# Performance work log

Hardware: AMD Instinct MI355X
Metric: run time of the kernel (lower is better)

The kernel has to match this reference:

```python
import jax, jax.numpy as jnp
import numpy as np

IN_DIM, DIM, H, L, B, N = 20, 128, 8, 3, 2, 192
DH = DIM // H
EPS = 1e-5


def _conv1d(x, w):
    # x: [b, Cin, n], w: [Cout, Cin, 3], pad=1
    return jax.lax.conv_general_dilated(x, w, (1,), [(1, 1)], dimension_numbers=('NCH', 'OIH', 'NCH'))


def _conv2d(x, w):
    # x: [b, Cin, n, n], w: [Cout, Cin, 3, 3], pad=1
    return jax.lax.conv_general_dilated(x, w, (1, 1), [(1, 1), (1, 1)], dimension_numbers=('NCHW', 'OIHW', 'NCHW'))


def _bn(x, g, b, axes):
    # BatchNorm in training mode (batch statistics, biased variance), channel axis = 1
    m = jnp.mean(x, axes, keepdims=True)
    v = jnp.var(x, axes, keepdims=True)
    sh = [1] * x.ndim
    sh[1] = -1
    return (x - m) / jnp.sqrt(v + EPS) * g.reshape(sh) + b.reshape(sh)


def _ln(x, g, b):
    m = jnp.mean(x, -1, keepdims=True)
    v = jnp.var(x, -1, keepdims=True)
    return (x - m) / jnp.sqrt(v + EPS) * g + b


def _seq2pair(c):
    # c: [b, C, n] -> [b, 2C, n, n]; first C channels constant over j, second C constant over i
    b, C, n = c.shape
    a = jnp.broadcast_to(c[:, :, :, None], (b, C, n, n))
    p = jnp.broadcast_to(c[:, :, None, :], (b, C, n, n))
    return jnp.concatenate([a, p], axis=1)


def _forward(seq, mask, conv1_w, conv2_w, ln_g, ln_b, c1d_w, bn1_g, bn1_b, c2d_w, bn2_g, bn2_b,
             wq_w, wq_b, wk_w, wk_b, wv_w, wv_b, wd_w, wd_b, wl_w, wl_b, fc_w, fc_b):
    b, n, _ = seq.shape
    s = seq.transpose(0, 2, 1)                    # [b, in_dim, n]
    x = _conv1d(s, conv1_w).transpose(0, 2, 1)    # [b, n, dim]
    c = _conv1d(s, conv2_w)                       # [b, dim, n]
    c2 = _seq2pair(c)                             # [b, 2*dim, n, n]
    scale = jnp.sqrt(jnp.asarray(DH, x.dtype))
    m4 = mask[:, None, None, :]                   # [b, 1, 1, n]
    for i in range(L):
        c = jax.nn.relu(_bn(_conv1d(c, c1d_w[i]), bn1_g[i], bn1_b[i], (0, 2)))
        x = _ln(x + c.transpose(0, 2, 1), ln_g[i], ln_b[i])
        c2 = c2 + _seq2pair(c)
        c2 = jax.nn.relu(_bn(_conv2d(c2, c2d_w[i]), bn2_g[i], bn2_b[i], (0, 2, 3)))
        dsym = c2 + c2.transpose(0, 1, 3, 2)      # symmetric pair features [b, 2*dim, n, n]
        gate = jax.nn.sigmoid(jnp.einsum('bcij,hc->bhij', dsym, wd_w[i]) + wd_b[i][None, :, None, None])
        heads = lambda y: y.reshape(b, n, H, DH).transpose(0, 2, 1, 3)
        q = heads(jax.nn.relu(x @ wq_w[i].T + wq_b[i]))
        k = heads(jax.nn.relu(x @ wk_w[i].T + wk_b[i]))
        v = heads(jax.nn.relu(x @ wv_w[i].T + wv_b[i]))
        a = jnp.einsum('bhid,bhjd->bhij', q, k) / scale
        e = jnp.exp(a - jnp.max(a, -1, keepdims=True)) * m4   # hand-rolled masked softmax
        attn = e / (jnp.sum(e, -1, keepdims=True) + 1e-6)
        attn = attn * gate                        # post-softmax multiplicative pair bias
        upd = jnp.einsum('bhij,bhjd->bhid', attn, v).transpose(0, 2, 1, 3).reshape(b, n, DIM)
        x = jax.nn.relu((x + upd) @ wl_w[i].T + wl_b[i])   # dropout = identity (eval)
    return jax.nn.relu(x @ fc_w.T + fc_b)


def setup_inputs():
    key = jax.random.key(0)
    ks = jax.random.split(key, 16)
    rn = lambda k, shape, s=0.05: jax.random.normal(k, shape, jnp.float32) * s
    C2 = 2 * DIM
    return {
        'seq': jax.random.normal(ks[0], (B, N, IN_DIM), jnp.float32),
        'mask': (jax.random.uniform(ks[1], (B, N)) > 0.1).astype(jnp.float32),
        'conv1_w': rn(ks[2], (DIM, IN_DIM, 3)),
        'conv2_w': rn(ks[3], (DIM, IN_DIM, 3)),
        'ln_g': jnp.ones((L, DIM), jnp.float32),
        'ln_b': jnp.zeros((L, DIM), jnp.float32),
        'c1d_w': rn(ks[4], (L, DIM, DIM, 3)),
        'bn1_g': jnp.ones((L, DIM), jnp.float32),
        'bn1_b': jnp.zeros((L, DIM), jnp.float32),
        'c2d_w': rn(ks[5], (L, C2, C2, 3, 3), 0.02),
        'bn2_g': jnp.ones((L, C2), jnp.float32),
        'bn2_b': jnp.zeros((L, C2), jnp.float32),
        'wq_w': rn(ks[6], (L, DIM, DIM)), 'wq_b': jnp.zeros((L, DIM), jnp.float32),
        'wk_w': rn(ks[7], (L, DIM, DIM)), 'wk_b': jnp.zeros((L, DIM), jnp.float32),
        'wv_w': rn(ks[8], (L, DIM, DIM)), 'wv_b': jnp.zeros((L, DIM), jnp.float32),
        'wd_w': rn(ks[9], (L, H, C2)), 'wd_b': jnp.zeros((L, H), jnp.float32),
        'wl_w': rn(ks[10], (L, DIM, DIM)), 'wl_b': jnp.zeros((L, DIM), jnp.float32),
        'fc_w': rn(ks[11], (DIM, DIM)), 'fc_b': jnp.zeros((DIM,), jnp.float32),
    }


def reference(seq, mask, conv1_w, conv2_w, ln_g, ln_b, c1d_w, bn1_g, bn1_b, c2d_w, bn2_g, bn2_b,
              wq_w, wq_b, wk_w, wk_b, wv_w, wv_b, wd_w, wd_b, wl_w, wl_b, fc_w, fc_b):
    return _forward(seq, mask, conv1_w, conv2_w, ln_g, ln_b, c1d_w, bn1_g, bn1_b, c2d_w, bn2_g, bn2_b,
                    wq_w, wq_b, wk_w, wk_b, wv_w, wv_b, wd_w, wd_b, wl_w, wl_b, fc_w, fc_b)
```

## Files before the change

kernel.cpp:

```cpp
#include <hip/hip_runtime.h>
#include <math.h>

#define IN_DIM 20
#define DIM 128
#define HH 8
#define LL 3
#define BB 2
#define NP 192
#define DHH 16
#define C2 256
#define NN (NP*NP)
#define EPS 1e-5f

#define PR 200
#define PC 224

typedef __bf16 bf16x8 __attribute__((ext_vector_type(8)));
typedef float  f32x16 __attribute__((ext_vector_type(16)));

union Pack8 { __bf16 h[8]; uint4 u; };

#define GLOAD16(gp, lp) \
  __builtin_amdgcn_global_load_lds((const __attribute__((address_space(1))) uint4*)(gp), \
                                   (__attribute__((address_space(3))) uint4*)(lp), 16, 0, 0)

__global__ void k_conv_init(const float* __restrict__ seq, const float* __restrict__ w1,
                            const float* __restrict__ w2, float* __restrict__ X,
                            float* __restrict__ Cc, float* __restrict__ CcT) {
  int t = blockIdx.x, b = blockIdx.y, oc = threadIdx.x;
  __shared__ float ss[3][IN_DIM];
  if (threadIdx.x < 3*IN_DIM) {
    int k = threadIdx.x / IN_DIM, ic = threadIdx.x % IN_DIM;
    int tt = t + k - 1;
    ss[k][ic] = (tt >= 0 && tt < NP) ? seq[(b*NP + tt)*IN_DIM + ic] : 0.f;
  }
  __syncthreads();
  float a1 = 0.f, a2 = 0.f;
  #pragma unroll
  for (int ic = 0; ic < IN_DIM; ic++) {
    #pragma unroll
    for (int k = 0; k < 3; k++) {
      float sv = ss[k][ic];
      a1 = fmaf(w1[(oc*IN_DIM + ic)*3 + k], sv, a1);
      a2 = fmaf(w2[(oc*IN_DIM + ic)*3 + k], sv, a2);
    }
  }
  X[(b*NP + t)*DIM + oc] = a1;
  Cc[(b*DIM + oc)*NP + t] = a2;
  CcT[(size_t)(b*NP + t)*DIM + oc] = a2;
}

__global__ __launch_bounds__(768)
void k_conv1d_bn_relu(const float* __restrict__ cin, const float* __restrict__ w,
                      const float* __restrict__ g, const float* __restrict__ bb,
                      float* __restrict__ cout, float* __restrict__ coutT) {
  int oc = blockIdx.x;
  int tid = threadIdx.x;
  int t = tid % NP;
  int sub = tid / NP;
  int b = sub & 1, ih = sub >> 1;
  float acc = 0.f;
  for (int ic = ih*64; ic < ih*64 + 64; ic++) {
    const float* cr = cin + (b*DIM + ic)*NP;
    const float* wr = w + (oc*DIM + ic)*3;
    float lf = (t > 0)      ? cr[t-1] : 0.f;
    float mf = cr[t];
    float rf = (t < NP-1)   ? cr[t+1] : 0.f;
    acc = fmaf(lf, wr[0], acc);
    acc = fmaf(mf, wr[1], acc);
    acc = fmaf(rf, wr[2], acc);
  }
  __shared__ float sp[4][NP];
  __shared__ float sb[768];
  sp[sub][t] = acc;
  __syncthreads();
  float raw = sp[b][t] + sp[2 + b][t];
  sb[tid] = (sub < 2) ? raw : raw * raw;
  __syncthreads();
  for (int s = 192; s >= 3; s >>= 1) {
    if (tid < s) sb[tid] += sb[tid + s];
    int u = tid - 384;
    if (u >= 0 && u < s) sb[tid] += sb[tid + s];
    __syncthreads();
  }
  float mean = (sb[0] + sb[1] + sb[2]) / 384.f;
  float var  = (sb[384] + sb[385] + sb[386]) / 384.f - mean*mean;
  float rstd = rsqrtf(var + EPS);
  if (sub < 2) {
    float v = fmaxf((raw - mean)*rstd*g[oc] + bb[oc], 0.f);
    cout[(b*DIM + oc)*NP + t] = v;
    coutT[(size_t)(b*NP + t)*DIM + oc] = v;
  }
}

__global__ void k_wtrans(const float* __restrict__ wq, const float* __restrict__ wk,
                         const float* __restrict__ wv, const float* __restrict__ wl,
                         const float* __restrict__ fcw,
                         float* __restrict__ wqt, float* __restrict__ wkt,
                         float* __restrict__ wvt, float* __restrict__ wlt,
                         float* __restrict__ fct) {
  int m = blockIdx.y;
  const float* src; float* dst;
  if (m < 3)       { src = wq + (size_t)m*DIM*DIM;     dst = wqt + (size_t)m*DIM*DIM; }
  else if (m < 6)  { src = wk + (size_t)(m-3)*DIM*DIM; dst = wkt + (size_t)(m-3)*DIM*DIM; }
  else if (m < 9)  { src = wv + (size_t)(m-6)*DIM*DIM; dst = wvt + (size_t)(m-6)*DIM*DIM; }
  else if (m < 12) { src = wl + (size_t)(m-9)*DIM*DIM; dst = wlt + (size_t)(m-9)*DIM*DIM; }
  else             { src = fcw;                        dst = fct; }
  int tile = blockIdx.x;
  int ti = tile >> 2, tj = tile & 3;
  int r = threadIdx.x >> 3, c4 = threadIdx.x & 7;
  __shared__ float t[32][33];
  float4 v = *(const float4*)(src + (ti*32 + r)*DIM + tj*32 + c4*4);
  t[r][c4*4+0] = v.x; t[r][c4*4+1] = v.y; t[r][c4*4+2] = v.z; t[r][c4*4+3] = v.w;
  __syncthreads();
  float4 o;
  o.x = t[c4*4+0][r]; o.y = t[c4*4+1][r]; o.z = t[c4*4+2][r]; o.w = t[c4*4+3][r];
  *(float4*)(dst + (tj*32 + r)*DIM + ti*32 + c4*4) = o;
}

__global__ __launch_bounds__(384)
void k_lnqkv(float* __restrict__ X, const float* __restrict__ ccT,
             const float* __restrict__ g, const float* __restrict__ bb,
             const float* __restrict__ wqt, const float* __restrict__ bq,
             const float* __restrict__ wkt, const float* __restrict__ bk,
             const float* __restrict__ wvt, const float* __restrict__ bv,
             float* __restrict__ Q, float* __restrict__ K, float* __restrict__ V) {
  int t = blockIdx.x, b = blockIdx.y;
  int tid = threadIdx.x;
  int lane = tid & 63, wave = tid >> 6;
  __shared__ float sy[DIM];
  __shared__ float sred[2];
  size_t o = (size_t)(b*NP + t)*DIM;
  float v = 0.f;
  if (tid < DIM) v = X[o + tid] + ccT[o + tid];
  if (tid < DIM) {
    float s = v;
    #pragma unroll
    for (int m = 32; m > 0; m >>= 1) s += __shfl_xor(s, m);
    if (lane == 0) sred[wave] = s;
  }
  __syncthreads();
  float mean = (sred[0] + sred[1]) * (1.f/128.f);
  float dv = v - mean;
  __syncthreads();
  if (tid < DIM) {
    float q = dv*dv;
    #pragma unroll
    for (int m = 32; m > 0; m >>= 1) q += __shfl_xor(q, m);
    if (lane == 0) sred[wave] = q;
  }
  __syncthreads();
  float var = (sred[0] + sred[1]) * (1.f/128.f);
  float rstd = rsqrtf(var + EPS);
  if (tid < DIM) {
    float xn = dv * rstd * g[tid] + bb[tid];
    X[o + tid] = xn;
    sy[tid] = xn;
  }
  __syncthreads();
  {
    int d2 = tid & 127, m = tid >> 7;
    const float* wt_m = (m == 0) ? wqt : (m == 1) ? wkt : wvt;
    const float* b_m  = (m == 0) ? bq  : (m == 1) ? bk  : bv;
    float* out_m      = (m == 0) ? Q   : (m == 1) ? K   : V;
    float acc = b_m[d2];
    for (int ee = 0; ee < DIM; ee++) acc = fmaf(wt_m[ee*DIM + d2], sy[ee], acc);
    int h = d2 >> 4, dh = d2 & 15;
    out_m[((size_t)(b*HH + h)*NP + t)*DHH + dh] = fmaxf(acc, 0.f);
  }
}

__global__ void k_wprep(const float* __restrict__ w, __bf16* __restrict__ wtb) {
  int l = blockIdx.x / C2, oc = blockIdx.x % C2;
  int tid = threadIdx.x;
  __shared__ float swt[C2*9];
  const float4* wsrc = (const float4*)(w + ((size_t)(l*C2 + oc))*C2*9);
  for (int idx = tid; idx < 576; idx += 256) ((float4*)swt)[idx] = wsrc[idx];
  __syncthreads();
  for (int v = tid; v < 288; v += 256) {
    int chunk = v / 18, rem = v % 18;
    int kk = rem >> 1, kh = rem & 1;
    Pack8 p;
    #pragma unroll
    for (int e = 0; e < 8; e++)
      p.h[e] = (__bf16)swt[(chunk*16 + kh*8 + e)*9 + kk];
    size_t unit = ((((size_t)(l*16 + chunk)*9 + kk)*2 + kh)*256 + oc);
    ((uint4*)wtb)[unit] = p.u;
  }
}

__global__ void k_make_convin(const float* __restrict__ CcT, const float* __restrict__ CLT0,
                              __bf16* __restrict__ inb, float* __restrict__ STATALL) {
  int idx = blockIdx.x*256 + threadIdx.x;
  if (blockIdx.x == 0) {
    for (int z = threadIdx.x; z < 3*2*C2; z += 256) STATALL[z] = 0.f;
  }
  int kh = idx & 1;
  int t = idx >> 1;
  int gcol = t % PC; int t2 = t / PC;
  int grow = t2 % PR; int t3 = t2 / PR;
  int chunk = t3 & 15; int b = t3 >> 4;
  int i = grow - 1, j = gcol - 8;
  Pack8 p;
  if ((unsigned)i < 192u && (unsigned)j < 192u) {
    int cbase = chunk*16 + kh*8;
    const float* pa;
    const float* pb;
    if (cbase < DIM) {
      pa = CcT  + (size_t)(b*NP + i)*DIM + cbase;
      pb = CLT0 + (size_t)(b*NP + i)*DIM + cbase;
    } else {
      pa = CcT  + (size_t)(b*NP + j)*DIM + (cbase - DIM);
      pb = CLT0 + (size_t)(b*NP + j)*DIM + (cbase - DIM);
    }
    #pragma unroll
    for (int e = 0; e < 8; e++) p.h[e] = (__bf16)(pa[e] + pb[e]);
  } else {
    #pragma unroll
    for (int e = 0; e < 8; e++) p.h[e] = (__bf16)0.f;
  }
  ((uint4*)inb)[idx] = p.u;
}

__global__ __launch_bounds__(256, 2)
void k_conv2d_mfma(const __bf16* __restrict__ inb,
                   const __bf16* __restrict__ wtb,
                   __bf16* __restrict__ rawb,
                   float* __restrict__ STAT2) {
  __shared__ __align__(16) uint4 sbuf[2*2176];
  int tid = threadIdx.x;
  int jt = blockIdx.x, it = blockIdx.y, zz = blockIdx.z;
  int b = zz >> 3, oct = zz & 7;
  int i0 = it*8, j0 = jt*64, oc0 = oct*32;
  int lane = tid & 63, wv = tid >> 6;
  int ln31 = lane & 31, khl = lane >> 5;

  const uint4* gW = (const uint4*)wtb;
  const uint4* gI = (const uint4*)inb;

  f32x16 acc[2][2];
  #pragma unroll
  for (int r = 0; r < 2; r++)
    #pragma unroll
    for (int n = 0; n < 2; n++)
      #pragma unroll
      for (int q = 0; q < 16; q++) acc[r][n][q] = 0.f;

  const uint4* gp[9];
  int lofs[9];
  int gstride[9];
  bool gvalid[9];
  #pragma unroll
  for (int t = 0; t < 9; t++) {
    int L = t*4 + wv;
    gvalid[t] = (L < 34);
    if (L < 9) {
      int u = L*64 + lane;
      int kkh = u >> 5;
      int ocl = u & 31;
      gp[t] = gW + (size_t)kkh*256 + oc0 + ocl;
      lofs[t] = u;
      gstride[t] = 4608;
    } else {
      int u = L*64 + lane - 576;
      int r = u / 160;
      int rem = u % 160;
      int kh = rem / 80;
      int c = rem % 80;
      gp[t] = gI + (((size_t)(b*16)*PR) + i0 + r)*PC*2 + (size_t)(j0 + c)*2 + kh;
      lofs[t] = 576 + u;
      gstride[t] = PR*PC*2;
    }
  }

  auto issue = [&](int buf) {
    uint4* lbase = sbuf + buf*2176;
    #pragma unroll
    for (int t = 0; t < 9; t++) {
      if (gvalid[t]) {
        GLOAD16(gp[t], lbase + lofs[t]);
        gp[t] += gstride[t];
      }
    }
  };

  issue(0);

  for (int chunk = 0; chunk < 16; ++chunk) {
    int buf = chunk & 1;
    __syncthreads();
    if (chunk < 15) issue(buf ^ 1);
    const __bf16* Wl = (const __bf16*)(sbuf + buf*2176);
    const __bf16* Il = (const __bf16*)(sbuf + buf*2176 + 576);
    #pragma unroll
    for (int kj = 0; kj < 3; kj++) {
      bf16x8 bfr[4][2];
      #pragma unroll
      for (int rr = 0; rr < 4; rr++) {
        int r = wv*2 + rr;
        #pragma unroll
        for (int ch = 0; ch < 2; ch++) {
          int c = ch*32 + ln31 + kj + 7;
          bfr[rr][ch] = *(const bf16x8*)(Il + ((r*2 + khl)*80 + c)*8);
        }
      }
      #pragma unroll
      for (int ki = 0; ki < 3; ki++) {
        int kk = ki*3 + kj;
        bf16x8 a = *(const bf16x8*)(Wl + ((kk*2 + khl)*32 + ln31)*8);
        #pragma unroll
        for (int row = 0; row < 2; row++)
          #pragma unroll
          for (int ch = 0; ch < 2; ch++)
            acc[row][ch] = __builtin_amdgcn_mfma_f32_32x32x16_bf16(a, bfr[row + ki][ch], acc[row][ch], 0, 0, 0);
      }
    }
  }

  __syncthreads();
  float* trAll = (float*)sbuf;
  float* tr = trAll + wv*(32*33);
  float* sstat = trAll + 4*32*33;
  if (tid < 64) sstat[tid] = 0.f;
  __syncthreads();

  #pragma unroll
  for (int reg = 0; reg < 16; reg++) {
    float v00 = acc[0][0][reg], v01 = acc[0][1][reg];
    float v10 = acc[1][0][reg], v11 = acc[1][1][reg];
    float s = v00 + v01 + v10 + v11;
    float s2 = v00*v00 + v01*v01 + v10*v10 + v11*v11;
    #pragma unroll
    for (int msk = 1; msk <= 16; msk <<= 1) { s += __shfl_xor(s, msk); s2 += __shfl_xor(s2, msk); }
    if (ln31 == 0) {
      int oc_l = (reg & 3) + 8*(reg >> 2) + 4*khl;
      atomicAdd(&sstat[oc_l], s);
      atomicAdd(&sstat[32 + oc_l], s2);
    }
  }

  int Gb = oc0 >> 3;
  uint4* RAWu = (uint4*)rawb;
  #pragma unroll
  for (int row = 0; row < 2; row++) {
    int i = i0 + wv*2 + row;
    #pragma unroll
    for (int ch = 0; ch < 2; ch++) {
      #pragma unroll
      for (int reg = 0; reg < 16; reg++) {
        int r = (reg & 3) + 8*(reg >> 2) + 4*khl;
        tr[r*33 + ln31] = acc[row][ch][reg];
      }
      __builtin_amdgcn_s_waitcnt(0);
      #pragma unroll
      for (int gs = 0; gs < 2; gs++) {
        int g = khl + gs*2;
        Pack8 p;
        #pragma unroll
        for (int e = 0; e < 8; e++) p.h[e] = (__bf16)tr[(g*8 + e)*33 + ln31];
        RAWu[((size_t)(b*32 + Gb + g)*192 + i)*192 + j0 + ch*32 + ln31] = p.u;
      }
      __builtin_amdgcn_s_waitcnt(0);
    }
  }

  __syncthreads();
  if (tid < 32) {
    atomicAdd(&STAT2[oc0 + tid], sstat[tid]);
    atomicAdd(&STAT2[C2 + oc0 + tid], sstat[32 + tid]);
  }
}

template<int WRITE_NEXT>
__global__ __launch_bounds__(768)
void k_bn2_norm_gate(const __bf16* __restrict__ rawb, const float* __restrict__ STAT2,
                     const float* __restrict__ g, const float* __restrict__ bb,
                     const float* __restrict__ wd, const float* __restrict__ CLnT,
                     __bf16* __restrict__ inb_next, float* __restrict__ tg) {
  int i = blockIdx.x, b = blockIdx.y;
  int tid = threadIdx.x;
  int j = tid % 192, qt = tid / 192;
  __shared__ float sscale[C2], sshift[C2], swd[HH*C2];
  __shared__ float sg[4][HH][192];
  const float inv = 1.f / (float)(BB*NN);
  for (int c = tid; c < C2; c += 768) {
    float mean = STAT2[c] * inv;
    float var  = STAT2[C2 + c] * inv - mean*mean;
    float rstd = rsqrtf(var + EPS);
    float sc = rstd * g[c];
    sscale[c] = sc;
    sshift[c] = bb[c] - mean*sc;
  }
  for (int idx = tid; idx < HH*C2; idx += 768) swd[idx] = wd[idx];
  __syncthreads();
  float gacc[HH] = {};
  const uint4* RAWu = (const uint4*)rawb;
  const float* clrow_i = CLnT ? CLnT + (size_t)(b*NP + i)*DIM : nullptr;
  const float* clrow_j = CLnT ? CLnT + (size_t)(b*NP + j)*DIM : nullptr;
  for (int cu = qt*8; cu < qt*8 + 8; cu++) {
    Pack8 pr; pr.u = RAWu[((size_t)(b*32 + cu)*NP + i)*NP + j];
    Pack8 p;
    int cbase = cu*8;
    const float* clp = (WRITE_NEXT && cbase < DIM) ? clrow_i + cbase
                     : (WRITE_NEXT ? clrow_j + (cbase - DIM) : nullptr);
    #pragma unroll
    for (int e = 0; e < 8; e++) {
      int c = cbase + e;
      float v = (float)pr.h[e];
      v = fmaxf(fmaf(v, sscale[c], sshift[c]), 0.f);
      if (WRITE_NEXT) p.h[e] = (__bf16)(v + clp[e]);
      #pragma unroll
      for (int h = 0; h < HH; h++) gacc[h] = fmaf(v, swd[h*C2 + c], gacc[h]);
    }
    if (WRITE_NEXT) {
      size_t unit = ((((size_t)(b*16 + (cu>>1))*PR + (i+1))*PC + (j+8))*2 + (cu&1));
      ((uint4*)inb_next)[unit] = p.u;
    }
  }
  #pragma unroll
  for (int h = 0; h < HH; h++) sg[qt][h][j] = gacc[h];
  __syncthreads();
  if (qt == 0) {
    #pragma unroll
    for (int h = 0; h < HH; h++)
      tg[((size_t)(b*HH + h)*NP + i)*NP + j] = sg[0][h][j] + sg[1][h][j] + sg[2][h][j] + sg[3][h][j];
  }
}

__global__ void k_gate(const float* __restrict__ tg, const float* __restrict__ wdb,
                       float* __restrict__ gate) {
  int tile = blockIdx.x;
  int hb = blockIdx.y;
  int b = hb >> 3, h = hb & 7;
  size_t bh = (size_t)(b*HH + h);
  int ti = tile / 6, tj = tile % 6;
  int r = threadIdx.x >> 3, c4 = threadIdx.x & 7;
  __shared__ float tB[32][33];
  const float* base = tg + bh*NN;
  float4 vb = *(const float4*)(base + (tj*32 + r)*NP + ti*32 + c4*4);
  tB[r][c4*4+0] = vb.x; tB[r][c4*4+1] = vb.y; tB[r][c4*4+2] = vb.z; tB[r][c4*4+3] = vb.w;
  __syncthreads();
  float4 va = *(const float4*)(base + (ti*32 + r)*NP + tj*32 + c4*4);
  float bias = wdb[h];
  float4 o;
  o.x = 1.f / (1.f + expf(-(va.x + tB[c4*4+0][r] + bias)));
  o.y = 1.f / (1.f + expf(-(va.y + tB[c4*4+1][r] + bias)));
  o.z = 1.f / (1.f + expf(-(va.z + tB[c4*4+2][r] + bias)));
  o.w = 1.f / (1.f + expf(-(va.w + tB[c4*4+3][r] + bias)));
  *(float4*)(gate + bh*NN + (ti*32 + r)*NP + tj*32 + c4*4) = o;
}

template<int MODE>
__global__ __launch_bounds__(384)
void k_attnx(const float* __restrict__ Q, const float* __restrict__ K,
             const float* __restrict__ V, const float* __restrict__ gate,
             const float* __restrict__ mask,
             float* __restrict__ X,
             const float* __restrict__ wlt, const float* __restrict__ bl,
             const float* __restrict__ ccnT,
             const float* __restrict__ lng, const float* __restrict__ lnb,
             const float* __restrict__ wqt, const float* __restrict__ bq,
             const float* __restrict__ wkt, const float* __restrict__ bk,
             const float* __restrict__ wvt, const float* __restrict__ bv,
             float* __restrict__ Qn, float* __restrict__ Kn, float* __restrict__ Vn,
             const float* __restrict__ fct, const float* __restrict__ fb,
             float* __restrict__ out) {
  int i = blockIdx.x, b = blockIdx.y;
  int tid = threadIdx.x;
  int j = tid % 192, half = tid / 192;
  int lane = tid & 63, wave = tid >> 6;
  __shared__ float sq[DIM];
  __shared__ float sattn[HH][NP];
  __shared__ float spv[3][DIM];
  __shared__ float supd[DIM];
  __shared__ float sy[DIM];
  __shared__ float sxp[3][DIM];
  __shared__ float sredm[HH][3];
  __shared__ float sreds[HH][3];
  __shared__ float sred[2];
  float mk = mask[b*NP + j];

  if (tid < DIM) {
    int h = tid >> 4, d = tid & 15;
    sq[tid] = Q[(((size_t)(b*HH + h))*NP + i)*DHH + d];
  }
  __syncthreads();

  float a[4], gt[4];
  #pragma unroll
  for (int hh = 0; hh < 4; hh++) {
    int h = half*4 + hh;
    size_t bh = (size_t)(b*HH + h);
    const float4* kr = (const float4*)(K + (bh*NP + j)*DHH);
    const float4* qr = (const float4*)(sq + h*DHH);
    float acc = 0.f;
    #pragma unroll
    for (int q4 = 0; q4 < 4; q4++) {
      float4 qv = qr[q4], kv = kr[q4];
      acc = fmaf(qv.x, kv.x, acc); acc = fmaf(qv.y, kv.y, acc);
      acc = fmaf(qv.z, kv.z, acc); acc = fmaf(qv.w, kv.w, acc);
    }
    a[hh] = acc * 0.25f;
    gt[hh] = gate[(bh*NP + i)*NP + j];
  }
  #pragma unroll
  for (int hh = 0; hh < 4; hh++) {
    int h = half*4 + hh;
    float m = a[hh];
    #pragma unroll
    for (int s = 32; s > 0; s >>= 1) m = fmaxf(m, __shfl_xor(m, s));
    if (lane == 0) sredm[h][wave % 3] = m;
  }
  __syncthreads();
  float e[4];
  #pragma unroll
  for (int hh = 0; hh < 4; hh++) {
    int h = half*4 + hh;
    float amax = fmaxf(fmaxf(sredm[h][0], sredm[h][1]), sredm[h][2]);
    e[hh] = expf(a[hh] - amax) * mk;
    float ss = e[hh];
    #pragma unroll
    for (int s = 32; s > 0; s >>= 1) ss += __shfl_xor(ss, s);
    if (lane == 0) sreds[h][wave % 3] = ss;
  }
  __syncthreads();
  #pragma unroll
  for (int hh = 0; hh < 4; hh++) {
    int h = half*4 + hh;
    float denom = sreds[h][0] + sreds[h][1] + sreds[h][2] + 1e-6f;
    sattn[h][j] = (e[hh] / denom) * gt[hh];
  }
  __syncthreads();

  {
    int d = tid & 15, h2 = (tid >> 4) & 7, jseg = tid >> 7;
    size_t bh = (size_t)(b*HH + h2);
    float acc = 0.f;
    for (int jj = jseg*64; jj < jseg*64 + 64; jj++)
      acc = fmaf(sattn[h2][jj], V[(bh*NP + jj)*DHH + d], acc);
    spv[jseg][h2*DHH + d] = acc;
  }
  __syncthreads();
  if (tid < DIM) supd[tid] = spv[0][tid] + spv[1][tid] + spv[2][tid];
  __syncthreads();

  size_t o = (size_t)(b*NP + i)*DIM;
  if (tid < DIM) sy[tid] = X[o + tid] + supd[tid];
  __syncthreads();
  {
    int d2 = tid & 127, ks = tid >> 7;
    int e0 = ks*43, e1 = (ks == 2) ? 128 : e0 + 43;
    float acc = (ks == 0) ? bl[d2] : 0.f;
    for (int ee = e0; ee < e1; ee++) acc = fmaf(wlt[ee*DIM + d2], sy[ee], acc);
    sxp[ks][d2] = acc;
  }
  __syncthreads();
  float xr = 0.f;
  if (tid < DIM) xr = fmaxf(sxp[0][tid] + sxp[1][tid] + sxp[2][tid], 0.f);
  __syncthreads();

  if (MODE == 0) {
    float v = 0.f;
    if (tid < DIM) v = xr + ccnT[o + tid];
    if (tid < DIM) {
      float s = v;
      #pragma unroll
      for (int m = 32; m > 0; m >>= 1) s += __shfl_xor(s, m);
      if (lane == 0) sred[wave] = s;
    }
    __syncthreads();
    float mean = (sred[0] + sred[1]) * (1.f/128.f);
    float dv = v - mean;
    __syncthreads();
    if (tid < DIM) {
      float q = dv*dv;
      #pragma unroll
      for (int m = 32; m > 0; m >>= 1) q += __shfl_xor(q, m);
      if (lane == 0) sred[wave] = q;
    }
    __syncthreads();
    float var = (sred[0] + sred[1]) * (1.f/128.f);
    float rstd = rsqrtf(var + EPS);
    if (tid < DIM) {
      float xn = dv * rstd * lng[tid] + lnb[tid];
      X[o + tid] = xn;
      sy[tid] = xn;
    }
    __syncthreads();
    {
      int d2 = tid & 127, m = tid >> 7;
      const float* wt_m = (m == 0) ? wqt : (m == 1) ? wkt : wvt;
      const float* b_m  = (m == 0) ? bq  : (m == 1) ? bk  : bv;
      float* out_m      = (m == 0) ? Qn  : (m == 1) ? Kn  : Vn;
      float acc = b_m[d2];
      for (int ee = 0; ee < DIM; ee++) acc = fmaf(wt_m[ee*DIM + d2], sy[ee], acc);
      int h = d2 >> 4, dh = d2 & 15;
      out_m[((size_t)(b*HH + h)*NP + i)*DHH + dh] = fmaxf(acc, 0.f);
    }
  } else {
    if (tid < DIM) sy[tid] = xr;
    __syncthreads();
    {
      int d2 = tid & 127, ks = tid >> 7;
      int e0 = ks*43, e1 = (ks == 2) ? 128 : e0 + 43;
      float acc = (ks == 0) ? fb[d2] : 0.f;
      for (int ee = e0; ee < e1; ee++) acc = fmaf(fct[ee*DIM + d2], sy[ee], acc);
      sxp[ks][d2] = acc;
    }
    __syncthreads();
    if (tid < DIM)
      out[o + tid] = fmaxf(sxp[0][tid] + sxp[1][tid] + sxp[2][tid], 0.f);
  }
}

extern "C" void kernel_launch(void* const* d_in, const int* in_sizes, int n_in,
                              void* d_out, int out_size, void* d_ws, size_t ws_size,
                              hipStream_t stream) {
  const float* seq     = (const float*)d_in[0];
  const float* mask    = (const float*)d_in[1];
  const float* conv1_w = (const float*)d_in[2];
  const float* conv2_w = (const float*)d_in[3];
  const float* ln_g    = (const float*)d_in[4];
  const float* ln_b    = (const float*)d_in[5];
  const float* c1d_w   = (const float*)d_in[6];
  const float* bn1_g   = (const float*)d_in[7];
  const float* bn1_b   = (const float*)d_in[8];
  const float* c2d_w   = (const float*)d_in[9];
  const float* bn2_g   = (const float*)d_in[10];
  const float* bn2_b   = (const float*)d_in[11];
  const float* wq_w    = (const float*)d_in[12];
  const float* wq_b    = (const float*)d_in[13];
  const float* wk_w    = (const float*)d_in[14];
  const float* wk_b    = (const float*)d_in[15];
  const float* wv_w    = (const float*)d_in[16];
  const float* wv_b    = (const float*)d_in[17];
  const float* wd_w    = (const float*)d_in[18];
  const float* wd_b    = (const float*)d_in[19];
  const float* wl_w    = (const float*)d_in[20];
  const float* wl_b    = (const float*)d_in[21];
  const float* fc_w    = (const float*)d_in[22];
  const float* fc_b    = (const float*)d_in[23];
  float* out = (float*)d_out;

  float* ws = (float*)d_ws;
  float* X    = ws; ws += BB*NP*DIM;
  float* Cc   = ws; ws += BB*DIM*NP;
  float* CcT  = ws; ws += BB*DIM*NP;
  float* CL0  = ws; ws += BB*DIM*NP;
  float* CL1  = ws; ws += BB*DIM*NP;
  float* CL2  = ws; ws += BB*DIM*NP;
  float* CLT0 = ws; ws += BB*DIM*NP;
  float* CLT1 = ws; ws += BB*DIM*NP;
  float* CLT2 = ws; ws += BB*DIM*NP;
  float* Q0   = ws; ws += BB*NP*DIM;
  float* K0   = ws; ws += BB*NP*DIM;
  float* V0   = ws; ws += BB*NP*DIM;
  float* Q1   = ws; ws += BB*NP*DIM;
  float* K1   = ws; ws += BB*NP*DIM;
  float* V1   = ws; ws += BB*NP*DIM;
  float* TG   = ws; ws += (size_t)BB*HH*NN;
  float* GATE = ws; ws += (size_t)BB*HH*NN;
  float* WQT  = ws; ws += (size_t)LL*DIM*DIM;
  float* WKT  = ws; ws += (size_t)LL*DIM*DIM;
  float* WVT  = ws; ws += (size_t)LL*DIM*DIM;
  float* WLT  = ws; ws += (size_t)LL*DIM*DIM;
  float* FCT  = ws; ws += (size_t)DIM*DIM;
  float* STATALL = ws; ws += 3*2*C2;
  __bf16* RAW = (__bf16*)ws; ws += (size_t)BB*C2*NN/2;
  __bf16* INB = (__bf16*)ws; ws += (size_t)BB*16*PR*PC*2*16/4;
  __bf16* WTB = (__bf16*)ws; ws += (size_t)LL*C2*C2*9/2;

  k_wtrans<<<dim3(16, 13), 256, 0, stream>>>(wq_w, wk_w, wv_w, wl_w, fc_w,
                                             WQT, WKT, WVT, WLT, FCT);
  k_wprep<<<LL*C2, 256, 0, stream>>>(c2d_w, WTB);
  k_conv_init<<<dim3(NP, BB), DIM, 0, stream>>>(seq, conv1_w, conv2_w, X, Cc, CcT);
  k_conv1d_bn_relu<<<DIM, 768, 0, stream>>>(Cc,  c1d_w + 0*(size_t)DIM*DIM*3, bn1_g + 0*DIM, bn1_b + 0*DIM, CL0, CLT0);
  k_conv1d_bn_relu<<<DIM, 768, 0, stream>>>(CL0, c1d_w + 1*(size_t)DIM*DIM*3, bn1_g + 1*DIM, bn1_b + 1*DIM, CL1, CLT1);
  k_conv1d_bn_relu<<<DIM, 768, 0, stream>>>(CL1, c1d_w + 2*(size_t)DIM*DIM*3, bn1_g + 2*DIM, bn1_b + 2*DIM, CL2, CLT2);
  k_make_convin<<<(BB*16*PR*PC*2)/256, 256, 0, stream>>>(CcT, CLT0, INB, STATALL);
  k_lnqkv<<<dim3(NP, BB), 384, 0, stream>>>(X, CLT0, ln_g, ln_b,
                                            WQT, wq_b, WKT, wk_b, WVT, wv_b, Q0, K0, V0);

  k_conv2d_mfma<<<dim3(3, 24, 16), 256, 0, stream>>>(INB, WTB + 0*(size_t)16*9*2*256*8, RAW, STATALL + 0*2*C2);
  k_bn2_norm_gate<1><<<dim3(NP, BB), 768, 0, stream>>>(RAW, STATALL + 0*2*C2, bn2_g + 0*C2, bn2_b + 0*C2,
                                                       wd_w + 0*(size_t)HH*C2, CLT1, INB, TG);
  k_gate<<<dim3(36, 16), 256, 0, stream>>>(TG, wd_b + 0*HH, GATE);
  k_attnx<0><<<dim3(NP, BB), 384, 0, stream>>>(Q0, K0, V0, GATE, mask, X,
                                               WLT + 0*(size_t)DIM*DIM, wl_b + 0*DIM,
                                               CLT1, ln_g + 1*DIM, ln_b + 1*DIM,
                                               WQT + 1*(size_t)DIM*DIM, wq_b + 1*DIM,
                                               WKT + 1*(size_t)DIM*DIM, wk_b + 1*DIM,
                                               WVT + 1*(size_t)DIM*DIM, wv_b + 1*DIM,
                                               Q1, K1, V1, nullptr, nullptr, nullptr);
  k_conv2d_mfma<<<dim3(3, 24, 16), 256, 0, stream>>>(INB, WTB + 1*(size_t)16*9*2*256*8, RAW, STATALL + 1*2*C2);
  k_bn2_norm_gate<1><<<dim3(NP, BB), 768, 0, stream>>>(RAW, STATALL + 1*2*C2, bn2_g + 1*C2, bn2_b + 1*C2,
                                                       wd_w + 1*(size_t)HH*C2, CLT2, INB, TG);
  k_gate<<<dim3(36, 16), 256, 0, stream>>>(TG, wd_b + 1*HH, GATE);
  k_attnx<0><<<dim3(NP, BB), 384, 0, stream>>>(Q1, K1, V1, GATE, mask, X,
                                               WLT + 1*(size_t)DIM*DIM, wl_b + 1*DIM,
                                               CLT2, ln_g + 2*DIM, ln_b + 2*DIM,
                                               WQT + 2*(size_t)DIM*DIM, wq_b + 2*DIM,
                                               WKT + 2*(size_t)DIM*DIM, wk_b + 2*DIM,
                                               WVT + 2*(size_t)DIM*DIM, wv_b + 2*DIM,
                                               Q0, K0, V0, nullptr, nullptr, nullptr);
  k_conv2d_mfma<<<dim3(3, 24, 16), 256, 0, stream>>>(INB, WTB + 2*(size_t)16*9*2*256*8, RAW, STATALL + 2*2*C2);
  k_bn2_norm_gate<0><<<dim3(NP, BB), 768, 0, stream>>>(RAW, STATALL + 2*2*C2, bn2_g + 2*C2, bn2_b + 2*C2,
                                                       wd_w + 2*(size_t)HH*C2, nullptr, nullptr, TG);
  k_gate<<<dim3(36, 16), 256, 0, stream>>>(TG, wd_b + 2*HH, GATE);
  k_attnx<1><<<dim3(NP, BB), 384, 0, stream>>>(Q0, K0, V0, GATE, mask, X,
                                               WLT + 2*(size_t)DIM*DIM, wl_b + 2*DIM,
                                               nullptr, nullptr, nullptr,
                                               nullptr, nullptr, nullptr, nullptr, nullptr, nullptr,
                                               nullptr, nullptr, nullptr,
                                               FCT, fc_b, out);
}
```

Baseline: 575.7 us.

## Retile conv2d MFMA kernel to 64 output channels by 4 rows per block

```diff
diff --git a/kernel.cpp b/kernel.cpp
--- a/kernel.cpp
+++ b/kernel.cpp
@@ -222,61 +222,63 @@
   ((uint4*)inb)[idx] = p.u;
 }
 
-__global__ __launch_bounds__(256, 2)
+__global__ __launch_bounds__(128, 1)
 void k_conv2d_mfma(const __bf16* __restrict__ inb,
                    const __bf16* __restrict__ wtb,
                    __bf16* __restrict__ rawb,
                    float* __restrict__ STAT2) {
-  __shared__ __align__(16) uint4 sbuf[2*2176];
+  __shared__ __align__(16) uint4 sbuf[2*2112];
   int tid = threadIdx.x;
   int jt = blockIdx.x, it = blockIdx.y, zz = blockIdx.z;
-  int b = zz >> 3, oct = zz & 7;
-  int i0 = it*8, j0 = jt*64, oc0 = oct*32;
+  int b = zz >> 2, oct = zz & 3;
+  int i0 = it*4, j0 = jt*64, oc0 = oct*64;
   int lane = tid & 63, wv = tid >> 6;
   int ln31 = lane & 31, khl = lane >> 5;
 
   const uint4* gW = (const uint4*)wtb;
   const uint4* gI = (const uint4*)inb;
 
-  f32x16 acc[2][2];
+  f32x16 acc[2][2][2];
   #pragma unroll
   for (int r = 0; r < 2; r++)
     #pragma unroll
-    for (int n = 0; n < 2; n++)
+    for (int m = 0; m < 2; m++)
       #pragma unroll
-      for (int q = 0; q < 16; q++) acc[r][n][q] = 0.f;
-
-  const uint4* gp[9];
-  int lofs[9];
-  int gstride[9];
-  bool gvalid[9];
-  #pragma unroll
-  for (int t = 0; t < 9; t++) {
-    int L = t*4 + wv;
-    gvalid[t] = (L < 34);
-    if (L < 9) {
+      for (int n = 0; n < 2; n++)
+        #pragma unroll
+        for (int q = 0; q < 16; q++) acc[r][m][n][q] = 0.f;
+
+  const uint4* gp[17];
+  int lofs[17];
+  int gstride[17];
+  bool gvalid[17];
+  #pragma unroll
+  for (int t = 0; t < 17; t++) {
+    int L = t*2 + wv;
+    gvalid[t] = (L < 33);
+    if (L < 18) {
       int u = L*64 + lane;
-      int kkh = u >> 5;
-      int ocl = u & 31;
+      int kkh = u >> 6;
+      int ocl = u & 63;
       gp[t] = gW + (size_t)kkh*256 + oc0 + ocl;
       lofs[t] = u;
       gstride[t] = 4608;
     } else {
-      int u = L*64 + lane - 576;
+      int u = (L - 18)*64 + lane;
       int r = u / 160;
       int rem = u % 160;
       int kh = rem / 80;
       int c = rem % 80;
       gp[t] = gI + (((size_t)(b*16)*PR) + i0 + r)*PC*2 + (size_t)(j0 + c)*2 + kh;
-      lofs[t] = 576 + u;
+      lofs[t] = 1152 + u;
       gstride[t] = PR*PC*2;
     }
   }
 
   auto issue = [&](int buf) {
-    uint4* lbase = sbuf + buf*2176;
-    #pragma unroll
-    for (int t = 0; t < 9; t++) {
+    uint4* lbase = sbuf + buf*2112;
+    #pragma unroll
+    for (int t = 0; t < 17; t++) {
       if (gvalid[t]) {
         GLOAD16(gp[t], lbase + lofs[t]);
         gp[t] += gstride[t];
@@ -290,29 +292,33 @@
     int buf = chunk & 1;
     __syncthreads();
     if (chunk < 15) issue(buf ^ 1);
-    const __bf16* Wl = (const __bf16*)(sbuf + buf*2176);
-    const __bf16* Il = (const __bf16*)(sbuf + buf*2176 + 576);
+    const __bf16* Wl = (const __bf16*)(sbuf + buf*2112);
+    const __bf16* Il = (const __bf16*)(sbuf + buf*2112 + 1152);
     #pragma unroll
     for (int kj = 0; kj < 3; kj++) {
       bf16x8 bfr[4][2];
       #pragma unroll
-      for (int rr = 0; rr < 4; rr++) {
-        int r = wv*2 + rr;
+      for (int rx = 0; rx < 4; rx++) {
+        int r = wv*2 + rx;
         #pragma unroll
         for (int ch = 0; ch < 2; ch++) {
           int c = ch*32 + ln31 + kj + 7;
-          bfr[rr][ch] = *(const bf16x8*)(Il + ((r*2 + khl)*80 + c)*8);
+          bfr[rx][ch] = *(const bf16x8*)(Il + ((r*2 + khl)*80 + c)*8);
         }
       }
       #pragma unroll
       for (int ki = 0; ki < 3; ki++) {
         int kk = ki*3 + kj;
-        bf16x8 a = *(const bf16x8*)(Wl + ((kk*2 + khl)*32 + ln31)*8);
+        bf16x8 a0 = *(const bf16x8*)(Wl + ((kk*2 + khl)*64 +      ln31)*8);
+        bf16x8 a1 = *(const bf16x8*)(Wl + ((kk*2 + khl)*64 + 32 + ln31)*8);
         #pragma unroll
-        for (int row = 0; row < 2; row++)
+        for (int rr = 0; rr < 2; rr++) {
           #pragma unroll
-          for (int ch = 0; ch < 2; ch++)
-            acc[row][ch] = __builtin_amdgcn_mfma_f32_32x32x16_bf16(a, bfr[row + ki][ch], acc[row][ch], 0, 0, 0);
+          for (int ch = 0; ch < 2; ch++) {
+            acc[rr][0][ch] = __builtin_amdgcn_mfma_f32_32x32x16_bf16(a0, bfr[rr + ki][ch], acc[rr][0][ch], 0, 0, 0);
+            acc[rr][1][ch] = __builtin_amdgcn_mfma_f32_32x32x16_bf16(a1, bfr[rr + ki][ch], acc[rr][1][ch], 0, 0, 0);
+          }
+        }
       }
     }
   }
@@ -320,54 +326,60 @@
   __syncthreads();
   float* trAll = (float*)sbuf;
   float* tr = trAll + wv*(32*33);
-  float* sstat = trAll + 4*32*33;
-  if (tid < 64) sstat[tid] = 0.f;
-  __syncthreads();
-
-  #pragma unroll
-  for (int reg = 0; reg < 16; reg++) {
-    float v00 = acc[0][0][reg], v01 = acc[0][1][reg];
-    float v10 = acc[1][0][reg], v11 = acc[1][1][reg];
-    float s = v00 + v01 + v10 + v11;
-    float s2 = v00*v00 + v01*v01 + v10*v10 + v11*v11;
-    #pragma unroll
-    for (int msk = 1; msk <= 16; msk <<= 1) { s += __shfl_xor(s, msk); s2 += __shfl_xor(s2, msk); }
-    if (ln31 == 0) {
-      int oc_l = (reg & 3) + 8*(reg >> 2) + 4*khl;
-      atomicAdd(&sstat[oc_l], s);
-      atomicAdd(&sstat[32 + oc_l], s2);
-    }
-  }
-
-  int Gb = oc0 >> 3;
+  float* sstat = trAll + 2*32*33;
+  if (tid < 128) sstat[tid] = 0.f;
+  __syncthreads();
+
+  #pragma unroll
+  for (int om = 0; om < 2; om++) {
+    #pragma unroll
+    for (int reg = 0; reg < 16; reg++) {
+      float v00 = acc[0][om][0][reg], v01 = acc[0][om][1][reg];
+      float v10 = acc[1][om][0][reg], v11 = acc[1][om][1][reg];
+      float s = v00 + v01 + v10 + v11;
+      float s2 = v00*v00 + v01*v01 + v10*v10 + v11*v11;
+      #pragma unroll
+      for (int msk = 1; msk <= 16; msk <<= 1) { s += __shfl_xor(s, msk); s2 += __shfl_xor(s2, msk); }
+      if (ln31 == 0) {
+        int oc_l = om*32 + (reg & 3) + 8*(reg >> 2) + 4*khl;
+        atomicAdd(&sstat[oc_l], s);
+        atomicAdd(&sstat[64 + oc_l], s2);
+      }
+    }
+  }
+
   uint4* RAWu = (uint4*)rawb;
   #pragma unroll
-  for (int row = 0; row < 2; row++) {
-    int i = i0 + wv*2 + row;
-    #pragma unroll
-    for (int ch = 0; ch < 2; ch++) {
+  for (int rr = 0; rr < 2; rr++) {
+    int i = i0 + wv*2 + rr;
+    #pragma unroll
+    for (int om = 0; om < 2; om++) {
+      int Gb = (oc0 + om*32) >> 3;
       #pragma unroll
-      for (int reg = 0; reg < 16; reg++) {
-        int r = (reg & 3) + 8*(reg >> 2) + 4*khl;
-        tr[r*33 + ln31] = acc[row][ch][reg];
+      for (int ch = 0; ch < 2; ch++) {
+        #pragma unroll
+        for (int reg = 0; reg < 16; reg++) {
+          int r = (reg & 3) + 8*(reg >> 2) + 4*khl;
+          tr[r*33 + ln31] = acc[rr][om][ch][reg];
+        }
+        __builtin_amdgcn_s_waitcnt(0);
+        #pragma unroll
+        for (int gs = 0; gs < 2; gs++) {
+          int g = khl + gs*2;
+          Pack8 p;
+          #pragma unroll
+          for (int e = 0; e < 8; e++) p.h[e] = (__bf16)tr[(g*8 + e)*33 + ln31];
+          RAWu[((size_t)(b*32 + Gb + g)*192 + i)*192 + j0 + ch*32 + ln31] = p.u;
+        }
+        __builtin_amdgcn_s_waitcnt(0);
       }
-      __builtin_amdgcn_s_waitcnt(0);
-      #pragma unroll
-      for (int gs = 0; gs < 2; gs++) {
-        int g = khl + gs*2;
-        Pack8 p;
-        #pragma unroll
-        for (int e = 0; e < 8; e++) p.h[e] = (__bf16)tr[(g*8 + e)*33 + ln31];
-        RAWu[((size_t)(b*32 + Gb + g)*192 + i)*192 + j0 + ch*32 + ln31] = p.u;
-      }
-      __builtin_amdgcn_s_waitcnt(0);
-    }
-  }
-
-  __syncthreads();
-  if (tid < 32) {
+    }
+  }
+
+  __syncthreads();
+  if (tid < 64) {
     atomicAdd(&STAT2[oc0 + tid], sstat[tid]);
-    atomicAdd(&STAT2[C2 + oc0 + tid], sstat[32 + tid]);
+    atomicAdd(&STAT2[C2 + oc0 + tid], sstat[64 + tid]);
   }
 }
 
@@ -681,7 +693,7 @@
   k_lnqkv<<<dim3(NP, BB), 384, 0, stream>>>(X, CLT0, ln_g, ln_b,
                                             WQT, wq_b, WKT, wk_b, WVT, wv_b, Q0, K0, V0);
 
-  k_conv2d_mfma<<<dim3(3, 24, 16), 256, 0, stream>>>(INB, WTB + 0*(size_t)16*9*2*256*8, RAW, STATALL + 0*2*C2);
+  k_conv2d_mfma<<<dim3(3, 48, 8), 128, 0, stream>>>(INB, WTB + 0*(size_t)16*9*2*256*8, RAW, STATALL + 0*2*C2);
   k_bn2_norm_gate<1><<<dim3(NP, BB), 768, 0, stream>>>(RAW, STATALL + 0*2*C2, bn2_g + 0*C2, bn2_b + 0*C2,
                                                        wd_w + 0*(size_t)HH*C2, CLT1, INB, TG);
   k_gate<<<dim3(36, 16), 256, 0, stream>>>(TG, wd_b + 0*HH, GATE);
@@ -692,7 +704,7 @@
                                                WKT + 1*(size_t)DIM*DIM, wk_b + 1*DIM,
                                                WVT + 1*(size_t)DIM*DIM, wv_b + 1*DIM,
                                                Q1, K1, V1, nullptr, nullptr, nullptr);
-  k_conv2d_mfma<<<dim3(3, 24, 16), 256, 0, stream>>>(INB, WTB + 1*(size_t)16*9*2*256*8, RAW, STATALL + 1*2*C2);
+  k_conv2d_mfma<<<dim3(3, 48, 8), 128, 0, stream>>>(INB, WTB + 1*(size_t)16*9*2*256*8, RAW, STATALL + 1*2*C2);
   k_bn2_norm_gate<1><<<dim3(NP, BB), 768, 0, stream>>>(RAW, STATALL + 1*2*C2, bn2_g + 1*C2, bn2_b + 1*C2,
                                                        wd_w + 1*(size_t)HH*C2, CLT2, INB, TG);
   k_gate<<<dim3(36, 16), 256, 0, stream>>>(TG, wd_b + 1*HH, GATE);
@@ -703,7 +715,7 @@
                                                WKT + 2*(size_t)DIM*DIM, wk_b + 2*DIM,
                                                WVT + 2*(size_t)DIM*DIM, wv_b + 2*DIM,
                                                Q0, K0, V0, nullptr, nullptr, nullptr);
-  k_conv2d_mfma<<<dim3(3, 24, 16), 256, 0, stream>>>(INB, WTB + 2*(size_t)16*9*2*256*8, RAW, STATALL + 2*2*C2);
+  k_conv2d_mfma<<<dim3(3, 48, 8), 128, 0, stream>>>(INB, WTB + 2*(size_t)16*9*2*256*8, RAW, STATALL + 2*2*C2);
   k_bn2_norm_gate<0><<<dim3(NP, BB), 768, 0, stream>>>(RAW, STATALL + 2*2*C2, bn2_g + 2*C2, bn2_b + 2*C2,
                                                        wd_w + 2*(size_t)HH*C2, nullptr, nullptr, TG);
   k_gate<<<dim3(36, 16), 256, 0, stream>>>(TG, wd_b + 2*HH, GATE);
```

Measured after the change: 674.6 us. 17.2% more time.
